# Performance work log

Measured on AMD Instinct MI355X. Metric: run time of the kernel, lower is better.

The kernel has to match this reference:

```python
import jax, jax.numpy as jnp
import numpy as np

# dims
N, T, F, DEMO, H, NHEAD, K, GCN, FFN = 4096, 48, 76, 4, 252, 4, 10, 256, 128
D = H + DEMO          # 256, input dim to graph constructor / clustering / gcn
DK = D // NHEAD       # 64
TAU, MASK_P, LAMBDA_KL, LAMBDA_CL, PHI_INIT, ALPHA = 0.5, 0.1, 1.0, 1.0, 3.0 / N, 1.0


def setup_inputs() -> dict:
    key = jax.random.key(0)
    ks = jax.random.split(key, 16)
    s = 0.02
    return dict(
        x=jax.random.normal(ks[0], (N, T, F), jnp.float32),
        x_demo=jax.random.normal(ks[1], (N, DEMO), jnp.float32),
        sorted_length=jax.random.randint(ks[2], (N,), 1, T + 1),
        mask_edge=jax.random.uniform(ks[3], (N, N), jnp.float32),
        w_ih=jax.random.normal(ks[4], (3 * H, F), jnp.float32) * s,
        w_hh=jax.random.normal(ks[5], (3 * H, H), jnp.float32) * s,
        b_ih=jnp.zeros((3 * H,), jnp.float32),
        b_hh=jnp.zeros((3 * H,), jnp.float32),
        h0=jnp.zeros((H,), jnp.float32),
        wq=jax.random.normal(ks[6], (D, D), jnp.float32) * s,
        bq=jnp.zeros((D,), jnp.float32),
        wk=jax.random.normal(ks[7], (D, D), jnp.float32) * s,
        bk=jnp.zeros((D,), jnp.float32),
        wo=jax.random.normal(ks[8], (NHEAD,), jnp.float32) * s,
        bo=jnp.zeros((), jnp.float32),
        phi=jnp.float32(PHI_INIT),
        centers=jax.random.normal(ks[9], (K, D), jnp.float32),
        gcn_w=jax.random.normal(ks[10], (D, GCN), jnp.float32) * s,
        gcn_b=jnp.zeros((GCN,), jnp.float32),
        ffn_w=jax.random.normal(ks[11], (GCN, FFN), jnp.float32) * s,
        ffn_b=jnp.zeros((FFN,), jnp.float32),
        pre_w=jax.random.normal(ks[12], (GCN, 2), jnp.float32) * s,
        pre_b=jnp.zeros((2,), jnp.float32),
    )


def _forward(x, x_demo, sorted_length, mask_edge, w_ih, w_hh, b_ih, b_hh, h0,
             wq, bq, wk, bk, wo, bo, phi, centers, gcn_w, gcn_b,
             ffn_w, ffn_b, pre_w, pre_b):
    n = x.shape[0]

    # --- GRU over time (torch nn.GRU equations), scan over T ---
    def gru_step(h, xt):
        gi = xt @ w_ih.T + b_ih                     # [N, 3H]
        gh = h @ w_hh.T + b_hh
        ir, iz, inn = jnp.split(gi, 3, axis=-1)
        hr, hz, hn = jnp.split(gh, 3, axis=-1)
        r = jax.nn.sigmoid(ir + hr)
        zg = jax.nn.sigmoid(iz + hz)
        ng = jnp.tanh(inn + r * hn)
        h = (1.0 - zg) * ng + zg * h
        return h, h

    _, outs = jax.lax.scan(gru_step, jnp.broadcast_to(h0, (n, H)), jnp.swapaxes(x, 0, 1))
    idx = jnp.clip(sorted_length - 1, 0, T - 1)
    x_gru = outs[idx, jnp.arange(n)]                # last valid hidden state [N, H]
    x_star = jnp.concatenate([x_gru, x_demo], axis=1)  # [N, D]

    # --- GraphConstructor: multi-head attention adjacency ---
    q = (x_star @ wq.T + bq).reshape(n, NHEAD, DK)
    kk = (x_star @ wk.T + bk).reshape(n, NHEAD, DK)
    scores = jnp.einsum('nhd,mhd->nmh', q, kk) / np.sqrt(DK)  # [N, N, h]
    scores = scores @ wo + bo                                  # Wo: Linear(h, 1)
    attn = jax.nn.softmax(scores, axis=1)
    eye = jnp.eye(n, dtype=x.dtype)
    adj = jnp.where(attn >= phi, 1.0, 0.0) * (1.0 - eye)       # threshold, zero diag

    # --- Clustering: soft assignment around given centers (KMeans fit replaced
    #     by fixed cluster_layer parameter; same soft-assign / KLD math) ---
    d2 = jnp.sum((x_star[:, None, :] - centers[None]) ** 2, axis=-1)  # [N, K]
    qsoft = 1.0 / (1.0 + d2 / ALPHA)
    qsoft = qsoft / jnp.sum(qsoft, axis=1, keepdims=True)
    pdist = qsoft ** 2 / jnp.sum(qsoft, axis=0, keepdims=True)
    pdist = jax.lax.stop_gradient(pdist / jnp.sum(pdist, axis=1, keepdims=True))
    label = jnp.argmax(qsoft, axis=1)
    kl_loss = jnp.mean(jnp.sum(pdist * jnp.log(pdist / (qsoft + 1e-6)), axis=-1))

    # --- GCNConv on dense adjacency (sym-normalized with self loops) ---
    xw = x_star @ gcn_w

    def gcn(a):
        a_hat = a + eye
        dinv = 1.0 / jnp.sqrt(jnp.sum(a_hat, axis=1))
        return (dinv[:, None] * a_hat * dinv[None, :]) @ xw + gcn_b

    z = gcn(adj)
    adj_aug = adj * (mask_edge >= MASK_P).astype(x.dtype)  # DataAug edge mask (bernoulli keep 1-p)
    z_aug = gcn(adj_aug)
    zf = z @ ffn_w + ffn_b
    zfa = z_aug @ ffn_w + ffn_b

    # --- clloss: NxN contrastive loss ---
    def l2n(a):
        return a / jnp.clip(jnp.linalg.norm(a, axis=1, keepdims=True), 1e-12, None)

    zn, zan = l2n(zf), l2n(zfa)
    intra = jnp.exp(zn @ zn.T / TAU)
    inter = jnp.exp(zn @ zan.T / TAU)
    cadj = (label[:, None] == label[None, :]).astype(x.dtype) * (1.0 - eye)
    cadj_new = jnp.where(adj == 1.0, 0.0, cadj)
    positive = jnp.diag(inter) + jnp.sum(intra * adj, axis=1) + jnp.sum(intra * cadj_new, axis=1)
    denom = jnp.sum(intra, axis=1) + jnp.sum(inter, axis=1) - jnp.diag(intra)
    cnt = jnp.sum(adj, axis=1) + jnp.sum(cadj_new, axis=1) + 1.0
    cl_loss = -jnp.sum(jnp.log(positive / denom) / cnt)

    loss = LAMBDA_KL * kl_loss + LAMBDA_CL * cl_loss
    output = z @ pre_w + pre_b
    return output, loss


def reference(x, x_demo, sorted_length, mask_edge, w_ih, w_hh, b_ih, b_hh, h0,
              wq, bq, wk, bk, wo, bo, phi, centers, gcn_w, gcn_b,
              ffn_w, ffn_b, pre_w, pre_b):
    return _forward(x, x_demo, sorted_length, mask_edge, w_ih, w_hh, b_ih, b_hh, h0,
                    wq, bq, wk, bk, wo, bo, phi, centers, gcn_w, gcn_b,
                    ffn_w, ffn_b, pre_w, pre_b)
```

## Files before the change

### kernel.cpp

```cpp
#include <hip/hip_runtime.h>
#include <cstdint>
#include <cstddef>

typedef _Float16 f16;
typedef f16 f16x8 __attribute__((ext_vector_type(8)));
typedef float f32x4 __attribute__((ext_vector_type(4)));

#define MFMA(a,b,c) __builtin_amdgcn_mfma_f32_16x16x32_f16(a,b,c,0,0,0)

__device__ __forceinline__ float sigm(float x){ return 1.f/(1.f+__expf(-x)); }
__device__ __forceinline__ float tanh_f(float x){
  float a = __expf(-2.f*fabsf(x));
  float t = (1.f-a)/(1.f+a);
  return x >= 0.f ? t : -t;
}
__device__ __forceinline__ uint16_t f2bf(float f){
  uint32_t u = __float_as_uint(f);
  return (uint16_t)((u + 0x7fffu + ((u>>16)&1u)) >> 16);
}
__device__ __forceinline__ float bf2f(uint16_t h){
  return __uint_as_float(((uint32_t)h) << 16);
}

__global__ __launch_bounds__(256) void k_prep(
    const float* __restrict__ w_ih, const float* __restrict__ w_hh,
    const float* __restrict__ b_ih, const float* __restrict__ b_hh,
    const int* __restrict__ slen,
    const float* __restrict__ wq, const float* __restrict__ wk,
    const float* __restrict__ gcn_w,
    f16* __restrict__ BgT, f16* __restrict__ wq16, f16* __restrict__ wk16,
    f16* __restrict__ gw16, float* __restrict__ biasc, int* __restrict__ idx)
{
  int id = blockIdx.x*256 + threadIdx.x;
  if (id < 360448){
    int g = id / (256*352); int rem = id % (256*352);
    int j = rem / 352; int k = rem % 352;
    float v = 0.f;
    if (j < 252){
      if (k < 96){
        if (k < 76 && g != 3){
          int row = (g==2) ? (504+j) : (g*252+j);
          v = w_ih[row*76 + k];
        }
      } else {
        int kh = k - 96;
        if (kh < 252 && g != 2){
          int row = (g==3) ? (504+j) : (g*252+j);
          v = w_hh[row*252 + kh];
        }
      }
    }
    BgT[id] = (f16)v;
    return;
  }
  id -= 360448;
  if (id < 65536){ wq16[id] = (f16)wq[id]; return; }
  id -= 65536;
  if (id < 65536){ wk16[id] = (f16)wk[id]; return; }
  id -= 65536;
  if (id < 65536){ int j = id >> 8, d = id & 255; gw16[id] = (f16)gcn_w[d*256 + j]; return; }
  id -= 65536;
  if (id < 1008){
    int g = id / 252, j = id % 252; float v;
    if (g==0) v = b_ih[j] + b_hh[j];
    else if (g==1) v = b_ih[252+j] + b_hh[252+j];
    else if (g==2) v = b_ih[504+j];
    else v = b_hh[504+j];
    biasc[id] = v; return;
  }
  id -= 1008;
  if (id < 4096){
    int s = slen[id] - 1; s = s < 0 ? 0 : (s > 47 ? 47 : s);
    idx[id] = s; return;
  }
}

__global__ __launch_bounds__(256) void k_xt(const float* __restrict__ x,
    f16* __restrict__ x16t)
{
  int id = blockIdx.x*256 + threadIdx.x;
  int c = id % 12; int rem = id / 12;
  int n = rem & 4095; int t = rem >> 12;
  const float* xp = x + ((size_t)n*48 + t)*76;
  f16x8 o;
  #pragma unroll
  for (int e = 0; e < 8; ++e){
    int k = c*8 + e;
    o[e] = (k < 76) ? (f16)xp[k] : (f16)0.f;
  }
  *(f16x8*)(x16t + ((size_t)t*4096 + n)*96 + c*8) = o;
}

__global__ __launch_bounds__(1024, 4) void k_gru_all(
    const f16* __restrict__ x16t, const f16* __restrict__ BgT,
    const float* __restrict__ biasc, const float* __restrict__ h0,
    const int* __restrict__ idxp, float* __restrict__ xstar,
    f16* __restrict__ xs16)
{
  __shared__ f16 hbuf[2][32][256];
  __shared__ int idxl[32];
  int lane = threadIdx.x & 63, w = threadIdx.x >> 6;
  int l16 = lane & 15, lq = lane >> 4;
  int nb = blockIdx.x * 32;

  for (int i = threadIdx.x; i < 32*256; i += 1024){
    int row = i >> 8, c = i & 255;
    int sc = (((c >> 3) ^ (row & 7)) << 3) | (c & 7);
    hbuf[0][row][sc] = (c < 252) ? (f16)h0[c] : (f16)0.f;
  }
  if (threadIdx.x < 32) idxl[threadIdx.x] = idxp[nb + threadIdx.x];

  int j = w*16 + l16;
  bool jv = (j < 252);
  int js = jv ? j : 251;
  float bR = biasc[js], bZ = biasc[252+js], bI = biasc[504+js], bH = biasc[756+js];
  const f16* pR = BgT + (size_t)(0*256 + j)*352 + lq*8;
  const f16* pZ = BgT + (size_t)(1*256 + j)*352 + lq*8;
  const f16* pI = BgT + (size_t)(2*256 + j)*352 + lq*8;
  const f16* pH = BgT + (size_t)(3*256 + j)*352 + lq*8;
  const f16* xp0 = x16t + ((size_t)nb + l16)*96 + lq*8;
  const f16* xp1 = x16t + ((size_t)nb + 16 + l16)*96 + lq*8;

  float hown[2][4];
  #pragma unroll
  for (int mf = 0; mf < 2; ++mf)
  #pragma unroll
  for (int r = 0; r < 4; ++r)
    hown[mf][r] = jv ? h0[js] : 0.f;

  __syncthreads();

  for (int t = 0; t < 48; ++t){
    const f16 (*hin)[256] = hbuf[t & 1];
    f16 (*hout)[256]      = hbuf[(t & 1) ^ 1];
    f32x4 z4 = {0.f,0.f,0.f,0.f};
    f32x4 aR[2] = {z4,z4}, aZ[2] = {z4,z4}, aI[2] = {z4,z4}, aH[2] = {z4,z4};
    size_t xt = (size_t)t*4096*96;

    f16x8 R0,Z0,M0, R1,Z1,M1, R2,Z2,M2, R3,Z3,M3;
#define PIN(s) asm volatile("" :: "v"(*(const f32x4*)&R##s), \
                                  "v"(*(const f32x4*)&Z##s), \
                                  "v"(*(const f32x4*)&M##s))
#define LW(s,u) do{ \
      R##s = *(const f16x8*)(pR + (u)*32); \
      Z##s = *(const f16x8*)(pZ + (u)*32); \
      M##s = *(const f16x8*)((((u) < 3) ? pI : pH) + (u)*32); \
      PIN(s); }while(0)
#define STEP(s,u) do{ \
      f16x8 a0, a1; \
      if ((u) < 3){ \
        a0 = *(const f16x8*)(xp0 + xt + (u)*32); \
        a1 = *(const f16x8*)(xp1 + xt + (u)*32); \
      } else { \
        int chunk = ((u) - 3)*4 + lq; \
        a0 = *(const f16x8*)(&hin[l16][(chunk ^ (l16 & 7)) << 3]); \
        a1 = *(const f16x8*)(&hin[16 + l16][(chunk ^ (l16 & 7)) << 3]); \
      } \
      aR[0] = MFMA(a0, R##s, aR[0]);  aR[1] = MFMA(a1, R##s, aR[1]); \
      aZ[0] = MFMA(a0, Z##s, aZ[0]);  aZ[1] = MFMA(a1, Z##s, aZ[1]); \
      if ((u) < 3){ aI[0] = MFMA(a0, M##s, aI[0]);  aI[1] = MFMA(a1, M##s, aI[1]); } \
      else        { aH[0] = MFMA(a0, M##s, aH[0]);  aH[1] = MFMA(a1, M##s, aH[1]); } \
    }while(0)

    LW(0,0); LW(1,1); LW(2,2); LW(3,3);
    STEP(0,0);   LW(0,4);
    STEP(1,1);   LW(1,5);
    STEP(2,2);   LW(2,6);
    STEP(3,3);   LW(3,7);
    STEP(0,4);   LW(0,8);
    STEP(1,5);   LW(1,9);
    STEP(2,6);   LW(2,10);
    STEP(3,7);
    STEP(0,8);
    STEP(1,9);
    STEP(2,10);
#undef LW
#undef STEP
#undef PIN

    #pragma unroll
    for (int mf = 0; mf < 2; ++mf)
    #pragma unroll
    for (int r = 0; r < 4; ++r){
      int row = mf*16 + lq*4 + r;
      float rr = sigm(aR[mf][r] + bR);
      float zz = sigm(aZ[mf][r] + bZ);
      float ng = tanh_f(aI[mf][r] + bI + rr*(aH[mf][r] + bH));
      float hnew = (1.f - zz)*ng + zz*hown[mf][r];
      hnew = jv ? hnew : 0.f;
      hown[mf][r] = hnew;
      int sc = (((j >> 3) ^ (row & 7)) << 3) | (j & 7);
      hout[row][sc] = (f16)hnew;
      if (jv && idxl[row] == t){
        xstar[((size_t)(nb + row) << 8) + j] = hnew;
        xs16[((size_t)(nb + row) << 8) + j] = (f16)hnew;
      }
    }
    __syncthreads();
  }
}

__global__ __launch_bounds__(256) void k_xdemo(const float* __restrict__ x_demo,
    float* __restrict__ xs32, f16* __restrict__ xs16)
{
  int id = blockIdx.x*256 + threadIdx.x;
  int n = id >> 2, c = id & 3;
  float v = x_demo[id];
  xs32[((size_t)n << 8) + 252 + c] = v;
  xs16[((size_t)n << 8) + 252 + c] = (f16)v;
}

template<int MODE>
__global__ __launch_bounds__(256) void k_proj(const f16* __restrict__ xs16,
    const f16* __restrict__ w16, const float* __restrict__ bias,
    const float* __restrict__ wo, f16* __restrict__ out16)
{
  int lane = threadIdx.x & 63, wv = threadIdx.x >> 6;
  int l16 = lane & 15, lq = lane >> 4;
  int nb = blockIdx.x * 64;
  int ocol = blockIdx.y*64 + wv*16 + l16;
  f32x4 z4 = {0.f,0.f,0.f,0.f};
  f32x4 acc[4] = {z4,z4,z4,z4};
  #pragma unroll
  for (int ks = 0; ks < 8; ++ks){
    f16x8 b = *(const f16x8*)(w16 + (size_t)ocol*256 + ks*32 + lq*8);
    #pragma unroll
    for (int mi = 0; mi < 4; ++mi){
      f16x8 a = *(const f16x8*)(xs16 + (size_t)(nb + mi*16 + l16)*256 + ks*32 + lq*8);
      acc[mi] = MFMA(a, b, acc[mi]);
    }
  }
  float badd = bias[ocol];
  float scale = (MODE == 0) ? wo[ocol >> 6]*0.125f : 1.f;
  #pragma unroll
  for (int mi = 0; mi < 4; ++mi)
  #pragma unroll
  for (int r = 0; r < 4; ++r){
    int n = nb + mi*16 + lq*4 + r;
    float v = acc[mi][r] + badd;
    if (MODE == 0) v *= scale;
    out16[(size_t)n*256 + ocol] = (f16)v;
  }
}

__global__ __launch_bounds__(256) void k_scores(const f16* __restrict__ qf,
    const f16* __restrict__ kf, uint16_t* __restrict__ sco)
{
  int lane = threadIdx.x & 63, w = threadIdx.x >> 6;
  int l16 = lane & 15, lq = lane >> 4;
  int mh = w >> 1, jh = w & 1;
  int nb = blockIdx.x*128 + mh*64;
  int mb = blockIdx.y*128 + jh*64;
  f32x4 z4 = {0.f,0.f,0.f,0.f};
  f32x4 acc[4][4];
  #pragma unroll
  for (int i = 0; i < 4; ++i)
  #pragma unroll
  for (int j = 0; j < 4; ++j) acc[i][j] = z4;
  #pragma unroll
  for (int ks = 0; ks < 8; ++ks){
    f16x8 a[4], b[4];
    #pragma unroll
    for (int i = 0; i < 4; ++i){
      a[i] = *(const f16x8*)(qf + (size_t)(nb + i*16 + l16)*256 + ks*32 + lq*8);
      b[i] = *(const f16x8*)(kf + (size_t)(mb + i*16 + l16)*256 + ks*32 + lq*8);
    }
    #pragma unroll
    for (int mi = 0; mi < 4; ++mi)
    #pragma unroll
    for (int jf = 0; jf < 4; ++jf)
      acc[mi][jf] = MFMA(a[mi], b[jf], acc[mi][jf]);
  }
  #pragma unroll
  for (int mi = 0; mi < 4; ++mi)
  #pragma unroll
  for (int jf = 0; jf < 4; ++jf)
  #pragma unroll
  for (int r = 0; r < 4; ++r){
    int n = nb + mi*16 + lq*4 + r;
    int m = mb + jf*16 + l16;
    sco[((size_t)n << 12) + m] = f2bf(acc[mi][jf][r]);
  }
}

__global__ __launch_bounds__(256) void k_adj(const uint16_t* __restrict__ sco,
    const float* __restrict__ mask_edge, const float* __restrict__ phip,
    uint8_t* __restrict__ flags, float* __restrict__ sadj,
    float* __restrict__ dinv, float* __restrict__ dinva)
{
  int n = blockIdx.x;
  int lane = threadIdx.x & 63, wv = threadIdx.x >> 6;
  const uint16_t* row = sco + ((size_t)n << 12);
  int base = threadIdx.x * 16;
  const uint4* p = (const uint4*)(row + base);
  uint4 w0 = p[0], w1 = p[1];
  uint32_t ws_[8] = {w0.x,w0.y,w0.z,w0.w,w1.x,w1.y,w1.z,w1.w};
  float v[16];
  #pragma unroll
  for (int i = 0; i < 8; ++i){
    v[2*i]   = bf2f((uint16_t)(ws_[i] & 0xffffu));
    v[2*i+1] = bf2f((uint16_t)(ws_[i] >> 16));
  }
  float mx = v[0];
  #pragma unroll
  for (int i = 1; i < 16; ++i) mx = fmaxf(mx, v[i]);
  #pragma unroll
  for (int o = 32; o >= 1; o >>= 1) mx = fmaxf(mx, __shfl_xor(mx, o));
  __shared__ float redA[4], redB[4], redC[4], redD[4];
  if (lane == 0) redA[wv] = mx;
  __syncthreads();
  mx = fmaxf(fmaxf(redA[0], redA[1]), fmaxf(redA[2], redA[3]));
  float s = 0.f;
  #pragma unroll
  for (int i = 0; i < 16; ++i) s += __expf(v[i] - mx);
  #pragma unroll
  for (int o = 32; o >= 1; o >>= 1) s += __shfl_xor(s, o);
  if (lane == 0) redB[wv] = s;
  __syncthreads();
  float rs = 1.f / (redB[0] + redB[1] + redB[2] + redB[3]);
  float phi = phip[0];
  uint32_t by[16]; int c0 = 0, c1 = 0;
  #pragma unroll
  for (int e = 0; e < 16; ++e){
    float a = __expf(v[e] - mx) * rs;
    int col = base + e;
    uint32_t b = (a >= phi && col != n) ? 1u : 0u;
    if (b){ if (mask_edge[((size_t)n << 12) + col] >= 0.1f) b |= 2u; }
    by[e] = b;
    c0 += (int)(b & 1u);
    c1 += (int)(b >> 1);
  }
  uint4 pk;
  pk.x = by[0]  | (by[1]  << 8) | (by[2]  << 16) | (by[3]  << 24);
  pk.y = by[4]  | (by[5]  << 8) | (by[6]  << 16) | (by[7]  << 24);
  pk.z = by[8]  | (by[9]  << 8) | (by[10] << 16) | (by[11] << 24);
  pk.w = by[12] | (by[13] << 8) | (by[14] << 16) | (by[15] << 24);
  *(uint4*)(flags + ((size_t)n << 12) + base) = pk;
  float f0 = (float)c0, f1 = (float)c1;
  #pragma unroll
  for (int o = 32; o >= 1; o >>= 1){ f0 += __shfl_xor(f0, o); f1 += __shfl_xor(f1, o); }
  if (lane == 0){ redC[wv] = f0; redD[wv] = f1; }
  __syncthreads();
  if (threadIdx.x == 0){
    float d0 = redC[0]+redC[1]+redC[2]+redC[3];
    float d1 = redD[0]+redD[1]+redD[2]+redD[3];
    sadj[n] = d0;
    dinv[n]  = rsqrtf(1.f + d0);
    dinva[n] = rsqrtf(1.f + d1);
  }
}

__global__ __launch_bounds__(256) void k_xw_y(const f16* __restrict__ xs16,
    const f16* __restrict__ gw16, const float* __restrict__ dinv,
    const float* __restrict__ dinva, f16* __restrict__ y16, f16* __restrict__ ya16)
{
  int lane = threadIdx.x & 63, wv = threadIdx.x >> 6;
  int l16 = lane & 15, lq = lane >> 4;
  int nb = blockIdx.x * 64;
  int jcol = blockIdx.y*64 + wv*16 + l16;
  f32x4 z4 = {0.f,0.f,0.f,0.f};
  f32x4 acc[4] = {z4,z4,z4,z4};
  #pragma unroll
  for (int ks = 0; ks < 8; ++ks){
    f16x8 b = *(const f16x8*)(gw16 + (size_t)jcol*256 + ks*32 + lq*8);
    #pragma unroll
    for (int mi = 0; mi < 4; ++mi){
      f16x8 a = *(const f16x8*)(xs16 + (size_t)(nb + mi*16 + l16)*256 + ks*32 + lq*8);
      acc[mi] = MFMA(a, b, acc[mi]);
    }
  }
  #pragma unroll
  for (int mi = 0; mi < 4; ++mi)
  #pragma unroll
  for (int r = 0; r < 4; ++r){
    int n = nb + mi*16 + lq*4 + r;
    float v = acc[mi][r];
    y16[(size_t)n*256 + jcol]  = (f16)(dinv[n]*v);
    ya16[(size_t)n*256 + jcol] = (f16)(dinva[n]*v);
  }
}

__global__ __launch_bounds__(256) void k_zgather(const uint8_t* __restrict__ flags,
    const f16* __restrict__ y16, const f16* __restrict__ ya16,
    const float* __restrict__ dinv, const float* __restrict__ dinva,
    const float* __restrict__ gcn_b, float* __restrict__ z32, float* __restrict__ za32)
{
  int n = blockIdx.x;
  int lane = threadIdx.x & 63, wv = threadIdx.x >> 6;
  uint4 w = ((const uint4*)(flags + ((size_t)n << 12)))[threadIdx.x];
  uint32_t m0[4] = {w.x & 0x01010101u, w.y & 0x01010101u, w.z & 0x01010101u, w.w & 0x01010101u};
  uint32_t m1[4] = {w.x & 0x02020202u, w.y & 0x02020202u, w.z & 0x02020202u, w.w & 0x02020202u};
  int c0 = __popc(m0[0]) + __popc(m0[1]) + __popc(m0[2]) + __popc(m0[3]);
  int c1 = __popc(m1[0]) + __popc(m1[1]) + __popc(m1[2]) + __popc(m1[3]);
  int v0 = c0, v1 = c1;
  #pragma unroll
  for (int o = 1; o < 64; o <<= 1){
    int u0 = __shfl_up(v0, o), u1 = __shfl_up(v1, o);
    if (lane >= o){ v0 += u0; v1 += u1; }
  }
  __shared__ int wsum0[4], wsum1[4];
  if (lane == 63){ wsum0[wv] = v0; wsum1[wv] = v1; }
  __syncthreads();
  int pos0 = v0 - c0, pos1 = v1 - c1;
  #pragma unroll
  for (int i = 0; i < 4; ++i) if (i < wv){ pos0 += wsum0[i]; pos1 += wsum1[i]; }
  int tot0 = wsum0[0]+wsum0[1]+wsum0[2]+wsum0[3];
  int tot1 = wsum1[0]+wsum1[1]+wsum1[2]+wsum1[3];
  __shared__ uint16_t list0[4096];
  __shared__ uint16_t list1[4096];
  int cbase = threadIdx.x * 16;
  #pragma unroll
  for (int q = 0; q < 4; ++q){
    uint32_t m = m0[q];
    while (m){
      int b = __ffs(m) - 1;
      list0[pos0++] = (uint16_t)(cbase + q*4 + (b >> 3));
      m &= m - 1;
    }
    m = m1[q];
    while (m){
      int b = __ffs(m) - 1;
      list1[pos1++] = (uint16_t)(cbase + q*4 + (b >> 3));
      m &= m - 1;
    }
  }
  __syncthreads();
  int j = threadIdx.x;
  float acc0 = (float)y16[((size_t)n << 8) + j];
  float acc1 = (float)ya16[((size_t)n << 8) + j];
  for (int i = 0; i < tot0; ++i) acc0 += (float)y16[((size_t)list0[i] << 8) + j];
  for (int i = 0; i < tot1; ++i) acc1 += (float)ya16[((size_t)list1[i] << 8) + j];
  z32[((size_t)n << 8) + j]  = dinv[n]*acc0 + gcn_b[j];
  za32[((size_t)n << 8) + j] = dinva[n]*acc1 + gcn_b[j];
}

__global__ __launch_bounds__(256) void k_cluster(const float* __restrict__ xs32,
    const float* __restrict__ centers, float* __restrict__ qsoft,
    int* __restrict__ labels, float* __restrict__ colsum)
{
  int nb = blockIdx.x * 16;
  __shared__ float xs[16][256];
  __shared__ float ct[2560];
  __shared__ float d2s[16][10];
  __shared__ float qs[16][10];
  for (int i = threadIdx.x; i < 16*256; i += 256) xs[i >> 8][i & 255] = xs32[(size_t)nb*256 + i];
  for (int i = threadIdx.x; i < 2560; i += 256){ int k = i >> 8, d = i & 255; ct[d*10 + k] = centers[i]; }
  __syncthreads();
  if (threadIdx.x < 160){
    int r = threadIdx.x / 10, k = threadIdx.x % 10;
    float s = 0.f;
    for (int d = 0; d < 256; ++d){ float df = xs[r][d] - ct[d*10 + k]; s += df*df; }
    d2s[r][k] = s;
  }
  __syncthreads();
  if (threadIdx.x < 16){
    int r = threadIdx.x;
    float un[10]; float tot = 0.f;
    #pragma unroll
    for (int k = 0; k < 10; ++k){ un[k] = 1.f/(1.f + d2s[r][k]); tot += un[k]; }
    float inv = 1.f / tot;
    int best = 0; float bm = un[0];
    #pragma unroll
    for (int k = 1; k < 10; ++k){ if (un[k] > bm){ bm = un[k]; best = k; } }
    labels[nb + r] = best;
    #pragma unroll
    for (int k = 0; k < 10; ++k){ float q = un[k]*inv; qs[r][k] = q; qsoft[(size_t)(nb + r)*10 + k] = q; }
  }
  __syncthreads();
  if (threadIdx.x < 10){
    int k = threadIdx.x; float s = 0.f;
    #pragma unroll
    for (int r = 0; r < 16; ++r) s += qs[r][k];
    atomicAdd(&colsum[k], s);
  }
}

__global__ __launch_bounds__(256) void k_kl(const float* __restrict__ qsoft,
    const float* __restrict__ colsum, float* __restrict__ klsum)
{
  int n = blockIdx.x*256 + threadIdx.x;
  float p[10]; float s = 0.f;
  #pragma unroll
  for (int k = 0; k < 10; ++k){
    float q = qsoft[(size_t)n*10 + k];
    float pu = q*q/colsum[k];
    p[k] = pu; s += pu;
  }
  float inv = 1.f/s; float kl = 0.f;
  #pragma unroll
  for (int k = 0; k < 10; ++k){
    float pk = p[k]*inv;
    float q = qsoft[(size_t)n*10 + k];
    kl += pk*__logf(pk/(q + 1e-6f));
  }
  int lane = threadIdx.x & 63, wv = threadIdx.x >> 6;
  #pragma unroll
  for (int o = 32; o >= 1; o >>= 1) kl += __shfl_xor(kl, o);
  __shared__ float red[4];
  if (lane == 0) red[wv] = kl;
  __syncthreads();
  if (threadIdx.x == 0) atomicAdd(klsum, red[0]+red[1]+red[2]+red[3]);
}

__global__ __launch_bounds__(128) void k_ffn(const float* __restrict__ z32,
    const float* __restrict__ za32, const float* __restrict__ ffn_w,
    const float* __restrict__ ffn_b, f16* __restrict__ zn16, f16* __restrict__ zan16)
{
  int n = blockIdx.x; int aug = blockIdx.y;
  const float* z = (aug ? za32 : z32) + ((size_t)n << 8);
  __shared__ float zr[256];
  zr[threadIdx.x] = z[threadIdx.x];
  zr[threadIdx.x + 128] = z[threadIdx.x + 128];
  __syncthreads();
  int j = threadIdx.x;
  float acc = ffn_b[j];
  #pragma unroll 8
  for (int d = 0; d < 256; ++d) acc += zr[d]*ffn_w[d*128 + j];
  float ss = acc*acc;
  int lane = threadIdx.x & 63, wv = threadIdx.x >> 6;
  #pragma unroll
  for (int o = 32; o >= 1; o >>= 1) ss += __shfl_xor(ss, o);
  __shared__ float sred[2];
  if (lane == 0) sred[wv] = ss;
  __syncthreads();
  float tot = sred[0] + sred[1];
  float rn = 1.f / fmaxf(sqrtf(tot), 1e-12f);
  (aug ? zan16 : zn16)[((size_t)n << 7) + j] = (f16)(acc*rn);
}

__global__ __launch_bounds__(256) void k_closs(const f16* __restrict__ zn,
    const f16* __restrict__ zan, const uint8_t* __restrict__ flags,
    const int* __restrict__ labels,
    float* __restrict__ rs1, float* __restrict__ rs2, float* __restrict__ rsA,
    float* __restrict__ rsC, float* __restrict__ rcC, float* __restrict__ rdI,
    float* __restrict__ rdi)
{
  int lane = threadIdx.x & 63;
  int ji = threadIdx.x >> 6;
  int l16 = lane & 15, lq = lane >> 4;
  int nb = blockIdx.x * 32;
  int mstart = blockIdx.y * 512;
  f16x8 A[2][4];
  #pragma unroll
  for (int mi = 0; mi < 2; ++mi)
  #pragma unroll
  for (int ks = 0; ks < 4; ++ks)
    A[mi][ks] = *(const f16x8*)(zn + (size_t)(nb + mi*16 + l16)*128 + ks*32 + lq*8);
  int labn[8];
  #pragma unroll
  for (int i = 0; i < 8; ++i) labn[i] = labels[nb + (i >> 2)*16 + lq*4 + (i & 3)];
  float a1[8]={}, a2[8]={}, aA[8]={}, aC[8]={}, aCc[8]={}, adI[8]={}, adi[8]={};
  uint8_t fA[8]; int labA;
  {
    int mcol0 = mstart + ji*16 + l16;
    #pragma unroll
    for (int i = 0; i < 8; ++i){
      int n = nb + (i >> 2)*16 + lq*4 + (i & 3);
      fA[i] = flags[((size_t)n << 12) + mcol0];
    }
    labA = labels[mcol0];
  }
  #pragma unroll
  for (int tile = 0; tile < 8; ++tile){
    int mcol = mstart + tile*64 + ji*16 + l16;
    uint8_t fB[8]; int labB = 0;
    if (tile < 7){
      int mn = mcol + 64;
      #pragma unroll
      for (int i = 0; i < 8; ++i){
        int n = nb + (i >> 2)*16 + lq*4 + (i & 3);
        fB[i] = flags[((size_t)n << 12) + mn];
      }
      labB = labels[mn];
    }
    f32x4 z4 = {0.f,0.f,0.f,0.f};
    f32x4 acc1[2] = {z4, z4};
    f32x4 acc2[2] = {z4, z4};
    #pragma unroll
    for (int ks = 0; ks < 4; ++ks){
      f16x8 b1 = *(const f16x8*)(zn  + (size_t)mcol*128 + ks*32 + lq*8);
      f16x8 b2 = *(const f16x8*)(zan + (size_t)mcol*128 + ks*32 + lq*8);
      #pragma unroll
      for (int mi = 0; mi < 2; ++mi){
        acc1[mi] = MFMA(A[mi][ks], b1, acc1[mi]);
        acc2[mi] = MFMA(A[mi][ks], b2, acc2[mi]);
      }
    }
    #pragma unroll
    for (int mi = 0; mi < 2; ++mi)
    #pragma unroll
    for (int r = 0; r < 4; ++r){
      int i8 = mi*4 + r;
      int n = nb + mi*16 + lq*4 + r;
      float e1 = __expf(2.f*acc1[mi][r]);
      float e2 = __expf(2.f*acc2[mi][r]);
      uint8_t fl = fA[i8];
      a1[i8] += e1; a2[i8] += e2;
      bool adjb = (fl & 1);
      if (adjb) aA[i8] += e1;
      if (!adjb && labn[i8] == labA && n != mcol){ aC[i8] += e1; aCc[i8] += 1.f; }
      if (n == mcol){ adI[i8] += e2; adi[i8] += e1; }
    }
    if (tile < 7){
      #pragma unroll
      for (int i = 0; i < 8; ++i) fA[i] = fB[i];
      labA = labB;
    }
  }
  #pragma unroll
  for (int i = 0; i < 8; ++i){
    #pragma unroll
    for (int o = 1; o < 16; o <<= 1){
      a1[i]  += __shfl_xor(a1[i], o);  a2[i]  += __shfl_xor(a2[i], o);
      aA[i]  += __shfl_xor(aA[i], o);  aC[i]  += __shfl_xor(aC[i], o);
      aCc[i] += __shfl_xor(aCc[i], o); adI[i] += __shfl_xor(adI[i], o);
      adi[i] += __shfl_xor(adi[i], o);
    }
  }
  if (l16 == 0){
    #pragma unroll
    for (int i = 0; i < 8; ++i){
      int n = nb + (i >> 2)*16 + lq*4 + (i & 3);
      atomicAdd(&rs1[n], a1[i]);  atomicAdd(&rs2[n], a2[i]);
      atomicAdd(&rsA[n], aA[i]);  atomicAdd(&rsC[n], aC[i]);
      atomicAdd(&rcC[n], aCc[i]); atomicAdd(&rdI[n], adI[i]);
      atomicAdd(&rdi[n], adi[i]);
    }
  }
}

__global__ __launch_bounds__(256) void k_clfinal(const float* __restrict__ rs1,
    const float* __restrict__ rs2, const float* __restrict__ rsA,
    const float* __restrict__ rsC, const float* __restrict__ rcC,
    const float* __restrict__ rdI, const float* __restrict__ rdi,
    const float* __restrict__ sadj, float* __restrict__ clsum)
{
  int n = blockIdx.x*256 + threadIdx.x;
  float pos = rdI[n] + rsA[n] + rsC[n];
  float den = rs1[n] + rs2[n] - rdi[n];
  float cnt = sadj[n] + rcC[n] + 1.f;
  float v = __logf(pos/den)/cnt;
  int lane = threadIdx.x & 63, wv = threadIdx.x >> 6;
  #pragma unroll
  for (int o = 32; o >= 1; o >>= 1) v += __shfl_xor(v, o);
  __shared__ float red[4];
  if (lane == 0) red[wv] = v;
  __syncthreads();
  if (threadIdx.x == 0) atomicAdd(clsum, red[0]+red[1]+red[2]+red[3]);
}

__global__ void k_loss(const float* __restrict__ scal, float* __restrict__ out){
  out[8192] = scal[0]*(1.f/4096.f) - scal[1];
}

__global__ __launch_bounds__(256) void k_outhead(const float* __restrict__ z32,
    const float* __restrict__ pre_w, const float* __restrict__ pre_b,
    float* __restrict__ out)
{
  int lane = threadIdx.x & 63, wv = threadIdx.x >> 6;
  int n = blockIdx.x*4 + wv;
  float4 zv = *(const float4*)(z32 + ((size_t)n << 8) + lane*4);
  float4 w0 = *(const float4*)(pre_w + lane*8);
  float4 w1 = *(const float4*)(pre_w + lane*8 + 4);
  float c0 = zv.x*w0.x + zv.y*w0.z + zv.z*w1.x + zv.w*w1.z;
  float c1 = zv.x*w0.y + zv.y*w0.w + zv.z*w1.y + zv.w*w1.w;
  #pragma unroll
  for (int o = 32; o >= 1; o >>= 1){ c0 += __shfl_xor(c0, o); c1 += __shfl_xor(c1, o); }
  if (lane == 0){
    out[(size_t)n*2]     = c0 + pre_b[0];
    out[(size_t)n*2 + 1] = c1 + pre_b[1];
  }
}

extern "C" void kernel_launch(void* const* d_in, const int* in_sizes, int n_in,
                              void* d_out, int out_size, void* d_ws, size_t ws_size,
                              hipStream_t stream)
{
  const float* x         = (const float*)d_in[0];
  const float* x_demo    = (const float*)d_in[1];
  const int*   slen      = (const int*)d_in[2];
  const float* mask_edge = (const float*)d_in[3];
  const float* w_ih      = (const float*)d_in[4];
  const float* w_hh      = (const float*)d_in[5];
  const float* b_ih      = (const float*)d_in[6];
  const float* b_hh      = (const float*)d_in[7];
  const float* h0        = (const float*)d_in[8];
  const float* wq        = (const float*)d_in[9];
  const float* bq        = (const float*)d_in[10];
  const float* wk        = (const float*)d_in[11];
  const float* bk        = (const float*)d_in[12];
  const float* wo        = (const float*)d_in[13];
  const float* phi       = (const float*)d_in[15];
  const float* centers   = (const float*)d_in[16];
  const float* gcn_w     = (const float*)d_in[17];
  const float* gcn_b     = (const float*)d_in[18];
  const float* ffn_w     = (const float*)d_in[19];
  const float* ffn_b     = (const float*)d_in[20];
  const float* pre_w     = (const float*)d_in[21];
  const float* pre_b     = (const float*)d_in[22];
  float* out = (float*)d_out;

  size_t off = 0;
  char* base = (char*)d_ws;
  auto take = [&](size_t bytes)->void*{
    void* p = base + off;
    off += (bytes + 255) & ~(size_t)255;
    return p;
  };
  f16*   BgT    = (f16*)take((size_t)4*256*352*2);
  f16*   wq16   = (f16*)take((size_t)65536*2);
  f16*   wk16   = (f16*)take((size_t)65536*2);
  f16*   gw16   = (f16*)take((size_t)65536*2);
  float* biasc  = (float*)take(1008*4);
  int*   idx    = (int*)take(4096*4);
  float* xs32   = (float*)take((size_t)4096*256*4);
  f16*   xs16   = (f16*)take((size_t)4096*256*2);
  f16*   qf16   = (f16*)take((size_t)4096*256*2);
  f16*   kf16   = (f16*)take((size_t)4096*256*2);
  uint16_t* sco = (uint16_t*)take((size_t)4096*4096*2);
  uint8_t* flags= (uint8_t*)take((size_t)4096*4096);
  float* sadj   = (float*)take(4096*4);
  float* dinv   = (float*)take(4096*4);
  float* dinva  = (float*)take(4096*4);
  f16*   y16    = (f16*)take((size_t)4096*256*2);
  f16*   ya16   = (f16*)take((size_t)4096*256*2);
  float* z32    = (float*)take((size_t)4096*256*4);
  float* za32   = (float*)take((size_t)4096*256*4);
  f16*   zn16   = (f16*)take((size_t)4096*128*2);
  f16*   zan16  = (f16*)take((size_t)4096*128*2);
  float* qsoft  = (float*)take((size_t)4096*10*4);
  int*   labels = (int*)take(4096*4);
  float* colsum = (float*)take(64);
  float* scal   = (float*)take(64);
  float* rsbuf  = (float*)take((size_t)7*4096*4);
  float* rs1 = rsbuf,        *rs2 = rsbuf + 4096, *rsA = rsbuf + 2*4096;
  float* rsC = rsbuf + 3*4096, *rcC = rsbuf + 4*4096;
  float* rdI = rsbuf + 5*4096, *rdi = rsbuf + 6*4096;

  f16* x16t = (f16*)sco;

  hipMemsetAsync(colsum, 0, 64, stream);
  hipMemsetAsync(scal, 0, 64, stream);
  hipMemsetAsync(rsbuf, 0, (size_t)7*4096*4, stream);

  k_prep<<<2196, 256, 0, stream>>>(w_ih, w_hh, b_ih, b_hh, slen, wq, wk, gcn_w,
                                   BgT, wq16, wk16, gw16, biasc, idx);
  k_xt<<<9216, 256, 0, stream>>>(x, x16t);
  k_xdemo<<<64, 256, 0, stream>>>(x_demo, xs32, xs16);
  k_gru_all<<<128, 1024, 0, stream>>>(x16t, BgT, biasc, h0, idx, xs32, xs16);
  k_proj<0><<<dim3(64, 4), 256, 0, stream>>>(xs16, wq16, bq, wo, qf16);
  k_proj<1><<<dim3(64, 4), 256, 0, stream>>>(xs16, wk16, bk, wo, kf16);
  k_scores<<<dim3(32, 32), 256, 0, stream>>>(qf16, kf16, sco);
  k_adj<<<4096, 256, 0, stream>>>(sco, mask_edge, phi, flags, sadj, dinv, dinva);
  k_xw_y<<<dim3(64, 4), 256, 0, stream>>>(xs16, gw16, dinv, dinva, y16, ya16);
  k_zgather<<<4096, 256, 0, stream>>>(flags, y16, ya16, dinv, dinva, gcn_b, z32, za32);
  k_cluster<<<256, 256, 0, stream>>>(xs32, centers, qsoft, labels, colsum);
  k_kl<<<16, 256, 0, stream>>>(qsoft, colsum, &scal[0]);
  k_ffn<<<dim3(4096, 2), 128, 0, stream>>>(z32, za32, ffn_w, ffn_b, zn16, zan16);
  k_closs<<<dim3(128, 8), 256, 0, stream>>>(zn16, zan16, flags, labels,
                                            rs1, rs2, rsA, rsC, rcC, rdI, rdi);
  k_clfinal<<<16, 256, 0, stream>>>(rs1, rs2, rsA, rsC, rcC, rdI, rdi, sadj, &scal[1]);
  k_loss<<<1, 1, 0, stream>>>(scal, out);
  k_outhead<<<1024, 256, 0, stream>>>(z32, pre_w, pre_b, out);

  (void)in_sizes; (void)n_in; (void)out_size; (void)ws_size;
}
```

Baseline: 874.7 us.

## Remap GRU waves to 16 rows by 32 columns with asm-pipelined weight loads

Each wave in the GRU recurrence kernel now covers 16 batch rows and two 16-column gate slices, where it used to cover 32 rows and one slice. The A fragment (x or h) is loaded once and reused across six MFMAs. Weight and x loads are issued through inline-asm global_load_dwordx4 with explicit vmcnt waits and double buffering, to hide global latency across the K loop. The cost is that each wave now loads twice as many weight bytes per step, and register pressure is higher.

Result: slower. 1.093 ms (+25.0%).

```diff
diff --git a/kernel.cpp b/kernel.cpp
--- a/kernel.cpp
+++ b/kernel.cpp
@@ -102,102 +102,118 @@
   int lane = threadIdx.x & 63, w = threadIdx.x >> 6;
   int l16 = lane & 15, lq = lane >> 4;
   int nb = blockIdx.x * 32;
+  int jg = w >> 1;
+  int rh = w & 1;
+  int row = rh*16 + l16;
 
   for (int i = threadIdx.x; i < 32*256; i += 1024){
-    int row = i >> 8, c = i & 255;
-    int sc = (((c >> 3) ^ (row & 7)) << 3) | (c & 7);
-    hbuf[0][row][sc] = (c < 252) ? (f16)h0[c] : (f16)0.f;
+    int rr_ = i >> 8, c = i & 255;
+    int sc = (((c >> 3) ^ (rr_ & 7)) << 3) | (c & 7);
+    hbuf[0][rr_][sc] = (c < 252) ? (f16)h0[c] : (f16)0.f;
   }
   if (threadIdx.x < 32) idxl[threadIdx.x] = idxp[nb + threadIdx.x];
 
-  int j = w*16 + l16;
-  bool jv = (j < 252);
-  int js = jv ? j : 251;
-  float bR = biasc[js], bZ = biasc[252+js], bI = biasc[504+js], bH = biasc[756+js];
-  const f16* pR = BgT + (size_t)(0*256 + j)*352 + lq*8;
-  const f16* pZ = BgT + (size_t)(1*256 + j)*352 + lq*8;
-  const f16* pI = BgT + (size_t)(2*256 + j)*352 + lq*8;
-  const f16* pH = BgT + (size_t)(3*256 + j)*352 + lq*8;
-  const f16* xp0 = x16t + ((size_t)nb + l16)*96 + lq*8;
-  const f16* xp1 = x16t + ((size_t)nb + 16 + l16)*96 + lq*8;
+  int j0 = jg*32 + l16;
+  int j1 = j0 + 16;
+  bool jv0 = (j0 < 252), jv1 = (j1 < 252);
+  int js0 = jv0 ? j0 : 251, js1 = jv1 ? j1 : 251;
+  float bRv[2] = {biasc[js0],     biasc[js1]};
+  float bZv[2] = {biasc[252+js0], biasc[252+js1]};
+  float bIv[2] = {biasc[504+js0], biasc[504+js1]};
+  float bHv[2] = {biasc[756+js0], biasc[756+js1]};
+
+  const f16* bR = BgT;
+  const f16* bZ = BgT + 90112;
+  const f16* bI = BgT + 180224;
+  const f16* bH = BgT + 270336;
+  int voff_w0 = (j0*352 + lq*8)*2;
+  int voff_w1 = (j1*352 + lq*8)*2;
+  int voff_x  = (row*96 + lq*8)*2;
 
   float hown[2][4];
   #pragma unroll
-  for (int mf = 0; mf < 2; ++mf)
+  for (int jf = 0; jf < 2; ++jf)
   #pragma unroll
   for (int r = 0; r < 4; ++r)
-    hown[mf][r] = jv ? h0[js] : 0.f;
-
-  __syncthreads();
+    hown[jf][r] = (jf ? jv1 : jv0) ? h0[jf ? js1 : js0] : 0.f;
+
+  __syncthreads();
+
+#define GLD(dst, vo, base, off) \
+  asm volatile("global_load_dwordx4 %0, %1, %2 offset:%3" \
+               : "=v"(dst) : "v"(vo), "s"(base), "n"(off) : "memory")
+#define WAITV(n) do{ \
+  asm volatile("s_waitcnt vmcnt(" #n ")" ::: "memory"); \
+  __builtin_amdgcn_sched_barrier(0); }while(0)
 
   for (int t = 0; t < 48; ++t){
     const f16 (*hin)[256] = hbuf[t & 1];
     f16 (*hout)[256]      = hbuf[(t & 1) ^ 1];
+    const f16* xb = x16t + (size_t)t*4096*96 + (size_t)nb*96;
     f32x4 z4 = {0.f,0.f,0.f,0.f};
     f32x4 aR[2] = {z4,z4}, aZ[2] = {z4,z4}, aI[2] = {z4,z4}, aH[2] = {z4,z4};
-    size_t xt = (size_t)t*4096*96;
-
-    f16x8 R0,Z0,M0, R1,Z1,M1, R2,Z2,M2, R3,Z3,M3;
-#define PIN(s) asm volatile("" :: "v"(*(const f32x4*)&R##s), \
-                                  "v"(*(const f32x4*)&Z##s), \
-                                  "v"(*(const f32x4*)&M##s))
-#define LW(s,u) do{ \
-      R##s = *(const f16x8*)(pR + (u)*32); \
-      Z##s = *(const f16x8*)(pZ + (u)*32); \
-      M##s = *(const f16x8*)((((u) < 3) ? pI : pH) + (u)*32); \
-      PIN(s); }while(0)
-#define STEP(s,u) do{ \
-      f16x8 a0, a1; \
-      if ((u) < 3){ \
-        a0 = *(const f16x8*)(xp0 + xt + (u)*32); \
-        a1 = *(const f16x8*)(xp1 + xt + (u)*32); \
-      } else { \
-        int chunk = ((u) - 3)*4 + lq; \
-        a0 = *(const f16x8*)(&hin[l16][(chunk ^ (l16 & 7)) << 3]); \
-        a1 = *(const f16x8*)(&hin[16 + l16][(chunk ^ (l16 & 7)) << 3]); \
-      } \
-      aR[0] = MFMA(a0, R##s, aR[0]);  aR[1] = MFMA(a1, R##s, aR[1]); \
-      aZ[0] = MFMA(a0, Z##s, aZ[0]);  aZ[1] = MFMA(a1, Z##s, aZ[1]); \
-      if ((u) < 3){ aI[0] = MFMA(a0, M##s, aI[0]);  aI[1] = MFMA(a1, M##s, aI[1]); } \
-      else        { aH[0] = MFMA(a0, M##s, aH[0]);  aH[1] = MFMA(a1, M##s, aH[1]); } \
+
+    f16x8 R0_0,R1_0,Z0_0,Z1_0,M0_0,M1_0,X_0;
+    f16x8 R0_1,R1_1,Z0_1,Z1_1,M0_1,M1_1,X_1;
+
+#define ISSU(s,u) do{ \
+      GLD(R0_##s, voff_w0, bR, (u)*64); GLD(R1_##s, voff_w1, bR, (u)*64); \
+      GLD(Z0_##s, voff_w0, bZ, (u)*64); GLD(Z1_##s, voff_w1, bZ, (u)*64); \
+      GLD(M0_##s, voff_w0, ((u) < 3) ? bI : bH, (u)*64); \
+      GLD(M1_##s, voff_w1, ((u) < 3) ? bI : bH, (u)*64); \
+      if ((u) < 3) GLD(X_##s, voff_x, xb, (u)*64); \
     }while(0)
-
-    LW(0,0); LW(1,1); LW(2,2); LW(3,3);
-    STEP(0,0);   LW(0,4);
-    STEP(1,1);   LW(1,5);
-    STEP(2,2);   LW(2,6);
-    STEP(3,3);   LW(3,7);
-    STEP(0,4);   LW(0,8);
-    STEP(1,5);   LW(1,9);
-    STEP(2,6);   LW(2,10);
-    STEP(3,7);
-    STEP(0,8);
-    STEP(1,9);
-    STEP(2,10);
-#undef LW
-#undef STEP
-#undef PIN
-
-    #pragma unroll
-    for (int mf = 0; mf < 2; ++mf)
-    #pragma unroll
-    for (int r = 0; r < 4; ++r){
-      int row = mf*16 + lq*4 + r;
-      float rr = sigm(aR[mf][r] + bR);
-      float zz = sigm(aZ[mf][r] + bZ);
-      float ng = tanh_f(aI[mf][r] + bI + rr*(aH[mf][r] + bH));
-      float hnew = (1.f - zz)*ng + zz*hown[mf][r];
-      hnew = jv ? hnew : 0.f;
-      hown[mf][r] = hnew;
-      int sc = (((j >> 3) ^ (row & 7)) << 3) | (j & 7);
-      hout[row][sc] = (f16)hnew;
-      if (jv && idxl[row] == t){
-        xstar[((size_t)(nb + row) << 8) + j] = hnew;
-        xs16[((size_t)(nb + row) << 8) + j] = (f16)hnew;
+#define STEPU(s,u) do{ \
+      f16x8 a; \
+      if ((u) < 3){ a = X_##s; } \
+      else { int chunk = ((u)-3)*4 + lq; \
+             a = *(const f16x8*)(&hin[row][(chunk ^ (l16 & 7)) << 3]); } \
+      aR[0] = MFMA(a, R0_##s, aR[0]);  aR[1] = MFMA(a, R1_##s, aR[1]); \
+      aZ[0] = MFMA(a, Z0_##s, aZ[0]);  aZ[1] = MFMA(a, Z1_##s, aZ[1]); \
+      if ((u) < 3){ aI[0] = MFMA(a, M0_##s, aI[0]);  aI[1] = MFMA(a, M1_##s, aI[1]); } \
+      else        { aH[0] = MFMA(a, M0_##s, aH[0]);  aH[1] = MFMA(a, M1_##s, aH[1]); } \
+    }while(0)
+
+    ISSU(0,0); ISSU(1,1);
+    WAITV(7);  STEPU(0,0);  ISSU(0,2);
+    WAITV(7);  STEPU(1,1);  ISSU(1,3);
+    WAITV(6);  STEPU(0,2);  ISSU(0,4);
+    WAITV(6);  STEPU(1,3);  ISSU(1,5);
+    WAITV(6);  STEPU(0,4);  ISSU(0,6);
+    WAITV(6);  STEPU(1,5);  ISSU(1,7);
+    WAITV(6);  STEPU(0,6);  ISSU(0,8);
+    WAITV(6);  STEPU(1,7);  ISSU(1,9);
+    WAITV(6);  STEPU(0,8);  ISSU(0,10);
+    WAITV(6);  STEPU(1,9);
+    WAITV(0);  STEPU(0,10);
+#undef ISSU
+#undef STEPU
+
+    #pragma unroll
+    for (int jf = 0; jf < 2; ++jf){
+      int jj  = jf ? j1 : j0;
+      bool jvv = jf ? jv1 : jv0;
+      #pragma unroll
+      for (int r = 0; r < 4; ++r){
+        int rown = rh*16 + lq*4 + r;
+        float rr = sigm(aR[jf][r] + bRv[jf]);
+        float zz = sigm(aZ[jf][r] + bZv[jf]);
+        float ng = tanh_f(aI[jf][r] + bIv[jf] + rr*(aH[jf][r] + bHv[jf]));
+        float hnew = (1.f - zz)*ng + zz*hown[jf][r];
+        hnew = jvv ? hnew : 0.f;
+        hown[jf][r] = hnew;
+        int sc = (((jj >> 3) ^ (rown & 7)) << 3) | (jj & 7);
+        hout[rown][sc] = (f16)hnew;
+        if (jvv && idxl[rown] == t){
+          xstar[((size_t)(nb + rown) << 8) + jj] = hnew;
+          xs16[((size_t)(nb + rown) << 8) + jj] = (f16)hnew;
+        }
       }
     }
     __syncthreads();
   }
+#undef GLD
+#undef WAITV
 }
 
 __global__ __launch_bounds__(256) void k_xdemo(const float* __restrict__ x_demo,
```

## Pre-swizzle GRU weights and inputs into MFMA fragment order for coalesced loads

Applied to the files above, without the earlier changes.

Weights are repacked into a fragment-major layout (per wave, per k-step, per gate, 64 lanes × 8 halves), dropping the zero-padded gate slots and shrinking the buffer. The time-major input is likewise stored in fragment order, so each lane's 16-byte load is contiguous across the wave. The hand-scheduled software-pipelined weight prefetch with asm register pinning is replaced by a plain unrolled loop, relying on the compiler to schedule the loads. The aim is fully coalesced global loads in the serial 48-step GRU, at the risk of losing the explicit load/MFMA overlap.

New measurement: 1.051 ms. +20.1%, slower.

```diff
diff --git a/kernel.cpp b/kernel.cpp
--- a/kernel.cpp
+++ b/kernel.cpp
@@ -28,32 +28,34 @@
     const int* __restrict__ slen,
     const float* __restrict__ wq, const float* __restrict__ wk,
     const float* __restrict__ gcn_w,
-    f16* __restrict__ BgT, f16* __restrict__ wq16, f16* __restrict__ wk16,
+    f16* __restrict__ BgF, f16* __restrict__ wq16, f16* __restrict__ wk16,
     f16* __restrict__ gw16, float* __restrict__ biasc, int* __restrict__ idx)
 {
   int id = blockIdx.x*256 + threadIdx.x;
-  if (id < 360448){
-    int g = id / (256*352); int rem = id % (256*352);
-    int j = rem / 352; int k = rem % 352;
+  if (id < 270336){
+    int e = id & 7;
+    int lane = (id >> 3) & 63;
+    int g = (id >> 9) % 3;
+    int rem = id / 1536;
+    int u = rem % 11;
+    int w = rem / 11;
+    int j = w*16 + (lane & 15);
+    int k = u*32 + ((lane >> 4) << 3) + e;
     float v = 0.f;
     if (j < 252){
-      if (k < 96){
-        if (k < 76 && g != 3){
-          int row = (g==2) ? (504+j) : (g*252+j);
-          v = w_ih[row*76 + k];
-        }
+      if (g < 2){
+        int row = (g == 0) ? j : (252 + j);
+        if (k < 76) v = w_ih[row*76 + k];
+        else if (k >= 96 && k < 348) v = w_hh[row*252 + (k - 96)];
       } else {
-        int kh = k - 96;
-        if (kh < 252 && g != 2){
-          int row = (g==3) ? (504+j) : (g*252+j);
-          v = w_hh[row*252 + kh];
-        }
+        if (u < 3){ if (k < 76) v = w_ih[(504+j)*76 + k]; }
+        else { int kh = k - 96; if (kh >= 0 && kh < 252) v = w_hh[(504+j)*252 + kh]; }
       }
     }
-    BgT[id] = (f16)v;
+    BgF[id] = (f16)v;
     return;
   }
-  id -= 360448;
+  id -= 270336;
   if (id < 65536){ wq16[id] = (f16)wq[id]; return; }
   id -= 65536;
   if (id < 65536){ wk16[id] = (f16)wk[id]; return; }
@@ -76,7 +78,7 @@
 }
 
 __global__ __launch_bounds__(256) void k_xt(const float* __restrict__ x,
-    f16* __restrict__ x16t)
+    f16* __restrict__ x16f)
 {
   int id = blockIdx.x*256 + threadIdx.x;
   int c = id % 12; int rem = id / 12;
@@ -88,11 +90,15 @@
     int k = c*8 + e;
     o[e] = (k < 76) ? (f16)xp[k] : (f16)0.f;
   }
-  *(f16x8*)(x16t + ((size_t)t*4096 + n)*96 + c*8) = o;
+  int u = c >> 2, lq = c & 3;
+  int nb = n >> 5, mf = (n >> 4) & 1, l16 = n & 15;
+  int lane = lq*16 + l16;
+  size_t dst = ((((size_t)t*128 + nb)*3 + u)*2 + mf)*512 + lane*8;
+  *(f16x8*)(x16f + dst) = o;
 }
 
 __global__ __launch_bounds__(1024, 4) void k_gru_all(
-    const f16* __restrict__ x16t, const f16* __restrict__ BgT,
+    const f16* __restrict__ x16f, const f16* __restrict__ BgF,
     const float* __restrict__ biasc, const float* __restrict__ h0,
     const int* __restrict__ idxp, float* __restrict__ xstar,
     f16* __restrict__ xs16)
@@ -114,13 +120,7 @@
   bool jv = (j < 252);
   int js = jv ? j : 251;
   float bR = biasc[js], bZ = biasc[252+js], bI = biasc[504+js], bH = biasc[756+js];
-  const f16* pR = BgT + (size_t)(0*256 + j)*352 + lq*8;
-  const f16* pZ = BgT + (size_t)(1*256 + j)*352 + lq*8;
-  const f16* pI = BgT + (size_t)(2*256 + j)*352 + lq*8;
-  const f16* pH = BgT + (size_t)(3*256 + j)*352 + lq*8;
-  const f16* xp0 = x16t + ((size_t)nb + l16)*96 + lq*8;
-  const f16* xp1 = x16t + ((size_t)nb + 16 + l16)*96 + lq*8;
-
+  const f16* pW = BgF + (size_t)w*(11*3*512) + lane*8;
   float hown[2][4];
   #pragma unroll
   for (int mf = 0; mf < 2; ++mf)
@@ -133,50 +133,29 @@
   for (int t = 0; t < 48; ++t){
     const f16 (*hin)[256] = hbuf[t & 1];
     f16 (*hout)[256]      = hbuf[(t & 1) ^ 1];
+    const f16* pX = x16f + (((size_t)t*128 + blockIdx.x)*6)*512 + lane*8;
     f32x4 z4 = {0.f,0.f,0.f,0.f};
     f32x4 aR[2] = {z4,z4}, aZ[2] = {z4,z4}, aI[2] = {z4,z4}, aH[2] = {z4,z4};
-    size_t xt = (size_t)t*4096*96;
-
-    f16x8 R0,Z0,M0, R1,Z1,M1, R2,Z2,M2, R3,Z3,M3;
-#define PIN(s) asm volatile("" :: "v"(*(const f32x4*)&R##s), \
-                                  "v"(*(const f32x4*)&Z##s), \
-                                  "v"(*(const f32x4*)&M##s))
-#define LW(s,u) do{ \
-      R##s = *(const f16x8*)(pR + (u)*32); \
-      Z##s = *(const f16x8*)(pZ + (u)*32); \
-      M##s = *(const f16x8*)((((u) < 3) ? pI : pH) + (u)*32); \
-      PIN(s); }while(0)
-#define STEP(s,u) do{ \
-      f16x8 a0, a1; \
-      if ((u) < 3){ \
-        a0 = *(const f16x8*)(xp0 + xt + (u)*32); \
-        a1 = *(const f16x8*)(xp1 + xt + (u)*32); \
-      } else { \
-        int chunk = ((u) - 3)*4 + lq; \
-        a0 = *(const f16x8*)(&hin[l16][(chunk ^ (l16 & 7)) << 3]); \
-        a1 = *(const f16x8*)(&hin[16 + l16][(chunk ^ (l16 & 7)) << 3]); \
-      } \
-      aR[0] = MFMA(a0, R##s, aR[0]);  aR[1] = MFMA(a1, R##s, aR[1]); \
-      aZ[0] = MFMA(a0, Z##s, aZ[0]);  aZ[1] = MFMA(a1, Z##s, aZ[1]); \
-      if ((u) < 3){ aI[0] = MFMA(a0, M##s, aI[0]);  aI[1] = MFMA(a1, M##s, aI[1]); } \
-      else        { aH[0] = MFMA(a0, M##s, aH[0]);  aH[1] = MFMA(a1, M##s, aH[1]); } \
-    }while(0)
-
-    LW(0,0); LW(1,1); LW(2,2); LW(3,3);
-    STEP(0,0);   LW(0,4);
-    STEP(1,1);   LW(1,5);
-    STEP(2,2);   LW(2,6);
-    STEP(3,3);   LW(3,7);
-    STEP(0,4);   LW(0,8);
-    STEP(1,5);   LW(1,9);
-    STEP(2,6);   LW(2,10);
-    STEP(3,7);
-    STEP(0,8);
-    STEP(1,9);
-    STEP(2,10);
-#undef LW
-#undef STEP
-#undef PIN
+
+    #pragma unroll
+    for (int u = 0; u < 11; ++u){
+      f16x8 wR = *(const f16x8*)(pW + ((u*3+0) << 9));
+      f16x8 wZ = *(const f16x8*)(pW + ((u*3+1) << 9));
+      f16x8 wM = *(const f16x8*)(pW + ((u*3+2) << 9));
+      f16x8 a0, a1;
+      if (u < 3){
+        a0 = *(const f16x8*)(pX + ((u*2+0) << 9));
+        a1 = *(const f16x8*)(pX + ((u*2+1) << 9));
+      } else {
+        int chunk = (u - 3)*4 + lq;
+        a0 = *(const f16x8*)(&hin[l16][(chunk ^ (l16 & 7)) << 3]);
+        a1 = *(const f16x8*)(&hin[16 + l16][(chunk ^ (l16 & 7)) << 3]);
+      }
+      aR[0] = MFMA(a0, wR, aR[0]);  aR[1] = MFMA(a1, wR, aR[1]);
+      aZ[0] = MFMA(a0, wZ, aZ[0]);  aZ[1] = MFMA(a1, wZ, aZ[1]);
+      if (u < 3){ aI[0] = MFMA(a0, wM, aI[0]);  aI[1] = MFMA(a1, wM, aI[1]); }
+      else      { aH[0] = MFMA(a0, wM, aH[0]);  aH[1] = MFMA(a1, wM, aH[1]); }
+    }
 
     #pragma unroll
     for (int mf = 0; mf < 2; ++mf)
@@ -707,7 +686,7 @@
     off += (bytes + 255) & ~(size_t)255;
     return p;
   };
-  f16*   BgT    = (f16*)take((size_t)4*256*352*2);
+  f16*   BgF    = (f16*)take((size_t)270336*2);
   f16*   wq16   = (f16*)take((size_t)65536*2);
   f16*   wk16   = (f16*)take((size_t)65536*2);
   f16*   gw16   = (f16*)take((size_t)65536*2);
@@ -737,17 +716,17 @@
   float* rsC = rsbuf + 3*4096, *rcC = rsbuf + 4*4096;
   float* rdI = rsbuf + 5*4096, *rdi = rsbuf + 6*4096;
 
-  f16* x16t = (f16*)sco;
+  f16* x16f = (f16*)sco;
 
   hipMemsetAsync(colsum, 0, 64, stream);
   hipMemsetAsync(scal, 0, 64, stream);
   hipMemsetAsync(rsbuf, 0, (size_t)7*4096*4, stream);
 
-  k_prep<<<2196, 256, 0, stream>>>(w_ih, w_hh, b_ih, b_hh, slen, wq, wk, gcn_w,
-                                   BgT, wq16, wk16, gw16, biasc, idx);
-  k_xt<<<9216, 256, 0, stream>>>(x, x16t);
+  k_prep<<<1844, 256, 0, stream>>>(w_ih, w_hh, b_ih, b_hh, slen, wq, wk, gcn_w,
+                                   BgF, wq16, wk16, gw16, biasc, idx);
+  k_xt<<<9216, 256, 0, stream>>>(x, x16f);
   k_xdemo<<<64, 256, 0, stream>>>(x_demo, xs32, xs16);
-  k_gru_all<<<128, 1024, 0, stream>>>(x16t, BgT, biasc, h0, idx, xs32, xs16);
+  k_gru_all<<<128, 1024, 0, stream>>>(x16f, BgF, biasc, h0, idx, xs32, xs16);
   k_proj<0><<<dim3(64, 4), 256, 0, stream>>>(xs16, wq16, bq, wo, qf16);
   k_proj<1><<<dim3(64, 4), 256, 0, stream>>>(xs16, wk16, bk, wo, kf16);
   k_scores<<<dim3(32, 32), 256, 0, stream>>>(qf16, kf16, sco);
```
